# Kernel tuning notes

Hardware: AMD Instinct MI355X
Metric: run time of the kernel (lower is better)

The kernel has to match this reference:

```python
import jax, jax.numpy as jnp
import numpy as np

V, E, H = 100000, 50, 64   # vocab, embedding dim, GRU hidden
B, T = 1024, 200           # batch, max playlist length


def setup_inputs() -> dict:
    key = jax.random.key(0)
    ks = jax.random.split(key, 12)
    ids = jax.random.randint(ks[0], (B, T), 1, V)
    lengths = jax.random.randint(ks[1], (B,), T // 4, T + 1)
    pos = jnp.arange(T)[None, :]
    input_tracks = jnp.where(pos < lengths[:, None], ids, 0)  # 0 = pad (mask_zero)
    s = 0.05
    p = lambda k, shp: jax.random.normal(k, shp, dtype=jnp.float32) * s
    z = lambda shp: jnp.zeros(shp, jnp.float32)
    return {
        "input_tracks": input_tracks,
        "emb": p(ks[2], (V, E)),
        "Wx_f": p(ks[3], (E, 3 * H)), "Wh_f": p(ks[4], (H, 3 * H)),
        "bi_f": z(3 * H), "br_f": z(3 * H),
        "Wx_b": p(ks[5], (E, 3 * H)), "Wh_b": p(ks[6], (H, 3 * H)),
        "bi_b": z(3 * H), "br_b": z(3 * H),
        "Wk": p(ks[7], (2 * H, H)), "bk": z(H),
        "Wq": p(ks[8], (H, H)), "bq": z(H),
        "We": p(ks[9], (H, 1)), "be": z(1),
    }


def _gru(x, mask, Wx, Wh, bi, br):
    """Keras GRU (reset_after=True) with masking; masked steps carry state.
    x: [B,T,E] float, mask: [B,T] bool. Returns (outputs [B,T,H], final state [B,H])."""
    gx = jnp.einsum('bte,eh->bth', x, Wx) + bi  # precompute input projections [B,T,3H]

    def step(h, inp):
        gxt, mt = inp                     # [B,3H], [B]
        gh = h @ Wh + br                  # [B,3H] recurrent projections (with recurrent bias)
        xz, xr, xh = jnp.split(gxt, 3, axis=-1)
        hz, hr, hn = jnp.split(gh, 3, axis=-1)
        zg = jax.nn.sigmoid(xz + hz)
        rg = jax.nn.sigmoid(xr + hr)
        hh = jnp.tanh(xh + rg * hn)
        h_new = zg * h + (1.0 - zg) * hh
        h_new = jnp.where(mt[:, None], h_new, h)  # carry state through padding
        return h_new, h_new

    h0 = jnp.zeros((x.shape[0], Wh.shape[0]), x.dtype)
    hT, outs = jax.lax.scan(step, h0, (gx.transpose(1, 0, 2), mask.T))
    return outs.transpose(1, 0, 2), hT


def reference(input_tracks, emb, Wx_f, Wh_f, bi_f, br_f, Wx_b, Wh_b, bi_b, br_b,
              Wk, bk, Wq, bq, We, be):
    mask = input_tracks != 0                       # [B,T]
    x = emb[input_tracks]                          # [B,T,E]
    out_f, h_f = _gru(x, mask, Wx_f, Wh_f, bi_f, br_f)
    out_b_rev, _ = _gru(x[:, ::-1], mask[:, ::-1], Wx_b, Wh_b, bi_b, br_b)
    out_b = out_b_rev[:, ::-1]
    out = jnp.concatenate([out_f, out_b], axis=-1)  # [B,T,2H]
    keys = out @ Wk + bk                            # [B,T,H]
    query = (h_f @ Wq + bq)[:, None, :]             # [B,1,H]
    energy = jnp.tanh(keys + query) @ We + be       # [B,T,1]
    energy = energy + (1.0 - mask.astype(jnp.float32))[:, :, None] * (-1e9)
    weights = jax.nn.softmax(energy, axis=1)        # softmax over time
    context = jnp.sum(weights * out, axis=1)        # [B,2H]
    return context
```

## Files before the change

kernel.cpp:

```cpp
#include <hip/hip_runtime.h>
#include <hip/hip_bf16.h>

#define VV 100000
#define EE 50
#define HH 64
#define BB 1024
#define TT 200

typedef float v4f __attribute__((ext_vector_type(4)));
typedef float f32x4 __attribute__((ext_vector_type(4)));
typedef short bf16x8 __attribute__((ext_vector_type(8)));

__device__ __forceinline__ float fsig(float x) {
    return 1.f / (1.f + __expf(-x));
}
__device__ __forceinline__ float ftanh(float x) {
    float e = __expf(2.f * x);
    return 1.f - 2.f / (e + 1.f);
}
__device__ __forceinline__ short f2bf(float f) {
    union { float f; unsigned u; } v; v.f = f;
    unsigned r = v.u + 0x7FFFu + ((v.u >> 16) & 1u);
    return (short)(r >> 16);
}

__global__ __launch_bounds__(256) void embw_kernel(
    const float* __restrict__ emb,
    const float* __restrict__ Wx_f, const float* __restrict__ bi_f,
    const float* __restrict__ Wx_b, const float* __restrict__ bi_b,
    float* __restrict__ embW_f, float* __restrict__ embW_b)
{
    const float* Wx = blockIdx.y ? Wx_b : Wx_f;
    const float* bi = blockIdx.y ? bi_b : bi_f;
    float* embW     = blockIdx.y ? embW_b : embW_f;
    __shared__ float wx_lds[EE * 192];
    __shared__ float emb_lds[32 * EE];
    const int tid = threadIdx.x;
    const int v0 = blockIdx.x * 32;
    for (int i = tid; i < EE * 192; i += 256) wx_lds[i] = Wx[i];
    for (int i = tid; i < 32 * EE; i += 256) emb_lds[i] = emb[(size_t)v0 * EE + i];
    __syncthreads();
    const int cg = tid & 63;
    const int rg = tid >> 6;
    float acc[8][3];
    #pragma unroll
    for (int i = 0; i < 8; i++) {
        acc[i][0] = bi[cg];
        acc[i][1] = bi[cg + 64];
        acc[i][2] = bi[cg + 128];
    }
    for (int k = 0; k < EE; k++) {
        const float wx0 = wx_lds[k * 192 + cg];
        const float wx1 = wx_lds[k * 192 + cg + 64];
        const float wx2 = wx_lds[k * 192 + cg + 128];
        #pragma unroll
        for (int i = 0; i < 8; i++) {
            const float ev = emb_lds[(rg * 8 + i) * EE + k];
            acc[i][0] = fmaf(ev, wx0, acc[i][0]);
            acc[i][1] = fmaf(ev, wx1, acc[i][1]);
            acc[i][2] = fmaf(ev, wx2, acc[i][2]);
        }
    }
    #pragma unroll
    for (int i = 0; i < 8; i++) {
        const size_t row = (size_t)(v0 + rg * 8 + i) * 192;
        embW[row + cg]       = acc[i][0];
        embW[row + cg + 64]  = acc[i][1];
        embW[row + cg + 128] = acc[i][2];
    }
}

__device__ __forceinline__ void opaque(v4f& x) {
    float a = x[0], b = x[1], c = x[2], d = x[3];
    asm volatile("" : "+v"(a), "+v"(b), "+v"(c), "+v"(d));
    x[0] = a; x[1] = b; x[2] = c; x[3] = d;
}
#define DECL_W(i) \
    v4f wz##i = {Wh[(4*i+0)*192+j],     Wh[(4*i+1)*192+j],     Wh[(4*i+2)*192+j],     Wh[(4*i+3)*192+j]};     \
    v4f wr##i = {Wh[(4*i+0)*192+64+j],  Wh[(4*i+1)*192+64+j],  Wh[(4*i+2)*192+64+j],  Wh[(4*i+3)*192+64+j]};  \
    v4f wn##i = {Wh[(4*i+0)*192+128+j], Wh[(4*i+1)*192+128+j], Wh[(4*i+2)*192+128+j], Wh[(4*i+3)*192+128+j]}; \
    opaque(wz##i); opaque(wr##i); opaque(wn##i);

#define GSTEP(i) { const v4f hv = h4[i]; \
    aZ = __builtin_elementwise_fma(hv, wz##i, aZ); \
    aR = __builtin_elementwise_fma(hv, wr##i, aR); \
    aN = __builtin_elementwise_fma(hv, wn##i, aN); }

__global__ __launch_bounds__(64, 2) void gru4_kernel(
    const int* __restrict__ ids,
    const float* __restrict__ embW_f, const float* __restrict__ embW_b,
    const float* __restrict__ Wh_f, const float* __restrict__ br_f,
    const float* __restrict__ Wh_b, const float* __restrict__ br_b,
    float* __restrict__ outb,
    float* __restrict__ hf_out)
{
    const int j   = threadIdx.x;
    const int b   = blockIdx.x;
    const int dir = blockIdx.y;
    const float* eW = dir ? embW_b : embW_f;
    const float* Wh = dir ? Wh_b : Wh_f;
    const float* br = dir ? br_b : br_f;

    DECL_W(0)  DECL_W(1)  DECL_W(2)  DECL_W(3)
    DECL_W(4)  DECL_W(5)  DECL_W(6)  DECL_W(7)
    DECL_W(8)  DECL_W(9)  DECL_W(10) DECL_W(11)
    DECL_W(12) DECL_W(13) DECL_W(14) DECL_W(15)
    const float brz = br[j], brr = br[64 + j], brn = br[128 + j];

    __shared__ __align__(16) float h_lds[64];
    __shared__ int ids_lds[TT];
    for (int i = j; i < TT; i += 64) ids_lds[i] = ids[(size_t)b * TT + i];
    h_lds[j] = 0.f;
    float hj = 0.f;
    __syncthreads();

    const int t0 = dir ? (TT - 1) : 0;
    const int dt = dir ? -1 : 1;

    int   id0 = ids_lds[t0];
    float gz0 = eW[(size_t)id0 * 192 + j];
    float gr0 = eW[(size_t)id0 * 192 + 64 + j];
    float gn0 = eW[(size_t)id0 * 192 + 128 + j];
    int   id1 = ids_lds[t0 + dt];
    float gz1 = eW[(size_t)id1 * 192 + j];
    float gr1 = eW[(size_t)id1 * 192 + 64 + j];
    float gn1 = eW[(size_t)id1 * 192 + 128 + j];

    float* obase = outb + (size_t)b * TT * 128 + dir * 64 + j;

    for (int s = 0; s < TT; s++) {
        const int t = t0 + s * dt;
        int id2 = 0; float gz2 = 0.f, gr2 = 0.f, gn2 = 0.f;
        if (s + 2 < TT) {
            id2 = ids_lds[t + 2 * dt];
            gz2 = eW[(size_t)id2 * 192 + j];
            gr2 = eW[(size_t)id2 * 192 + 64 + j];
            gn2 = eW[(size_t)id2 * 192 + 128 + j];
        }
        v4f aZ = {brz, 0.f, 0.f, 0.f};
        v4f aR = {brr, 0.f, 0.f, 0.f};
        v4f aN = {brn, 0.f, 0.f, 0.f};
        const v4f* h4 = (const v4f*)h_lds;
        GSTEP(0)  GSTEP(1)  GSTEP(2)  GSTEP(3)
        GSTEP(4)  GSTEP(5)  GSTEP(6)  GSTEP(7)
        GSTEP(8)  GSTEP(9)  GSTEP(10) GSTEP(11)
        GSTEP(12) GSTEP(13) GSTEP(14) GSTEP(15)
        const float az = (aZ[0] + aZ[1]) + (aZ[2] + aZ[3]);
        const float ar = (aR[0] + aR[1]) + (aR[2] + aR[3]);
        const float an = (aN[0] + aN[1]) + (aN[2] + aN[3]);
        const float z  = fsig(gz0 + az);
        const float r  = fsig(gr0 + ar);
        const float hh = ftanh(gn0 + r * an);
        float hnew = z * hj + (1.f - z) * hh;
        hnew = (id0 != 0) ? hnew : hj;
        hj = hnew;
        h_lds[j] = hj;
        obase[(size_t)t * 128] = hj;
        id0 = id1; gz0 = gz1; gr0 = gr1; gn0 = gn1;
        id1 = id2; gz1 = gz2; gr1 = gr2; gn1 = gn2;
    }
    if (dir == 0) hf_out[(size_t)b * 64 + j] = hj;
}

#define NTILE 13

__global__ __launch_bounds__(256) void attn7_kernel(
    const int* __restrict__ ids,
    const float* __restrict__ outb,
    const float* __restrict__ hf,
    const float* __restrict__ Wk, const float* __restrict__ bk,
    const float* __restrict__ Wq, const float* __restrict__ bq,
    const float* __restrict__ We, const float* __restrict__ be,
    float* __restrict__ ctx)
{
    __shared__ __align__(16) short wk_sw[1024 * 8];
    __shared__ float q_lds[64];
    __shared__ float we_lds[64];
    __shared__ float e_lds[TT];
    __shared__ float part[4][128];
    const int b = blockIdx.x;
    const int tid = threadIdx.x;
    const int w = tid >> 6;
    const int lane = tid & 63;
    const int l15 = lane & 15;
    const int lhi = lane >> 4;

    #pragma unroll
    for (int i = 0; i < 4; i++) {
        const int slot = tid + 256 * i;
        const int s_l15 = slot & 15;
        const int s_nt  = (slot >> 4) & 3;
        const int s_lhi = (slot >> 6) & 3;
        const int s_ks  = slot >> 8;
        const int kbase = 32 * s_ks + 8 * s_lhi;
        const int col   = 16 * s_nt + s_l15;
        bf16x8 v;
        #pragma unroll
        for (int jj = 0; jj < 8; jj++) v[jj] = f2bf(Wk[(size_t)(kbase + jj) * 64 + col]);
        *(bf16x8*)&wk_sw[slot * 8] = v;
    }
    if (tid < 64) {
        float qc = bq[tid];
        const float* hfb = hf + (size_t)b * 64;
        for (int k = 0; k < 64; k++) qc = fmaf(hfb[k], Wq[k * 64 + tid], qc);
        q_lds[tid] = qc;
        we_lds[tid] = We[tid];
    }
    __syncthreads();

    for (int tile = w; tile < NTILE; tile += 4) {
        const int t0 = tile * 16;
        const int t = t0 + l15;
        f32x4 acc[4];
        #pragma unroll
        for (int nt = 0; nt < 4; nt++) { acc[nt][0] = 0.f; acc[nt][1] = 0.f; acc[nt][2] = 0.f; acc[nt][3] = 0.f; }
        #pragma unroll
        for (int ks = 0; ks < 4; ks++) {
            bf16x8 a;
            if (t < TT) {
                const float* p = outb + ((size_t)b * TT + t) * 128 + 32 * ks + 8 * lhi;
                const float4 lo = *(const float4*)p;
                const float4 hi = *(const float4*)(p + 4);
                a[0] = f2bf(lo.x); a[1] = f2bf(lo.y); a[2] = f2bf(lo.z); a[3] = f2bf(lo.w);
                a[4] = f2bf(hi.x); a[5] = f2bf(hi.y); a[6] = f2bf(hi.z); a[7] = f2bf(hi.w);
            } else {
                #pragma unroll
                for (int jj = 0; jj < 8; jj++) a[jj] = 0;
            }
            #pragma unroll
            for (int nt = 0; nt < 4; nt++) {
                const bf16x8 bf = *(const bf16x8*)&wk_sw[(ks * 256 + lhi * 64 + nt * 16 + l15) * 8];
                acc[nt] = __builtin_amdgcn_mfma_f32_16x16x32_bf16(a, bf, acc[nt], 0, 0, 0);
            }
        }
        float ep0 = 0.f, ep1 = 0.f, ep2 = 0.f, ep3 = 0.f;
        #pragma unroll
        for (int nt = 0; nt < 4; nt++) {
            const int c = 16 * nt + l15;
            const float qn = q_lds[c];
            const float wen = we_lds[c];
            ep0 = fmaf(wen, ftanh(acc[nt][0] + qn), ep0);
            ep1 = fmaf(wen, ftanh(acc[nt][1] + qn), ep1);
            ep2 = fmaf(wen, ftanh(acc[nt][2] + qn), ep2);
            ep3 = fmaf(wen, ftanh(acc[nt][3] + qn), ep3);
        }
        #pragma unroll
        for (int off = 1; off < 16; off <<= 1) {
            ep0 += __shfl_xor(ep0, off);
            ep1 += __shfl_xor(ep1, off);
            ep2 += __shfl_xor(ep2, off);
            ep3 += __shfl_xor(ep3, off);
        }
        if (l15 == 0) {
            const int rbase = t0 + 4 * lhi;
            if (rbase + 0 < TT) e_lds[rbase + 0] = ep0;
            if (rbase + 1 < TT) e_lds[rbase + 1] = ep1;
            if (rbase + 2 < TT) e_lds[rbase + 2] = ep2;
            if (rbase + 3 < TT) e_lds[rbase + 3] = ep3;
        }
    }
    __syncthreads();
    if (w == 0) {
        const float bev = be[0];
        for (int t = lane; t < TT; t += 64) {
            float e = e_lds[t] + bev;
            if (ids[(size_t)b * TT + t] == 0) e -= 1e9f;
            e_lds[t] = e;
        }
        float m = -1e30f;
        for (int t = lane; t < TT; t += 64) m = fmaxf(m, e_lds[t]);
        #pragma unroll
        for (int off = 32; off > 0; off >>= 1) m = fmaxf(m, __shfl_xor(m, off));
        float ssum = 0.f;
        for (int t = lane; t < TT; t += 64) { const float v = __expf(e_lds[t] - m); e_lds[t] = v; ssum += v; }
        #pragma unroll
        for (int off = 32; off > 0; off >>= 1) ssum += __shfl_xor(ssum, off);
        const float inv = 1.f / ssum;
        for (int t = lane; t < TT; t += 64) e_lds[t] *= inv;
    }
    __syncthreads();
    float c0 = 0.f, c1 = 0.f;
    for (int t = w; t < TT; t += 4) {
        const float* orow = outb + ((size_t)b * TT + t) * 128;
        const float wt = e_lds[t];
        c0 = fmaf(wt, orow[lane], c0);
        c1 = fmaf(wt, orow[64 + lane], c1);
    }
    part[w][lane] = c0;
    part[w][64 + lane] = c1;
    __syncthreads();
    if (tid < 128)
        ctx[(size_t)b * 128 + tid] = part[0][tid] + part[1][tid] + part[2][tid] + part[3][tid];
}

template<bool USE_EMBW>
__global__ __launch_bounds__(192, 2) void gru_kernel(
    const int* __restrict__ ids,
    const float* __restrict__ embW_f, const float* __restrict__ embW_b,
    const float* __restrict__ emb,
    const float* __restrict__ Wx_f, const float* __restrict__ bi_f,
    const float* __restrict__ Wx_b, const float* __restrict__ bi_b,
    const float* __restrict__ Wh_f, const float* __restrict__ br_f,
    const float* __restrict__ Wh_b, const float* __restrict__ br_b,
    float* __restrict__ outb, float* __restrict__ hf_out)
{
    constexpr int R = 4;
    __shared__ float h_lds[R][64];
    __shared__ float rg_lds[R][64];
    __shared__ float hh_lds[R][64];
    __shared__ int ids_lds[R * TT];
    const int tid = threadIdx.x;
    const int w = tid >> 6;
    const int j = tid & 63;
    const int dir = blockIdx.y;
    const int b0 = blockIdx.x * R;
    const float* embW = dir ? embW_b : embW_f;
    const float* Wh   = dir ? Wh_b : Wh_f;
    const float* br   = dir ? br_b : br_f;
    const float* Wx   = dir ? Wx_b : Wx_f;
    const float* bi   = dir ? bi_b : bi_f;
    const int c = w * 64 + j;

    float whc[64];
    #pragma unroll
    for (int k = 0; k < 64; k++) whc[k] = Wh[k * 192 + c];
    const float brc = br[c];
    float wxc[EE];
    float bic = 0.f;
    if (!USE_EMBW) {
        #pragma unroll
        for (int k = 0; k < EE; k++) wxc[k] = Wx[k * 192 + c];
        bic = bi[c];
    }
    for (int i = tid; i < R * TT; i += 192) ids_lds[i] = ids[(size_t)b0 * TT + i];
    if (w == 0) {
        #pragma unroll
        for (int r = 0; r < R; r++) h_lds[r][j] = 0.f;
    }
    __syncthreads();

    for (int s = 0; s < TT; s++) {
        const int t = dir ? (TT - 1 - s) : s;
        int idv[R];
        float gxv[R], accv[R];
        #pragma unroll
        for (int r = 0; r < R; r++) idv[r] = ids_lds[r * TT + t];
        if (USE_EMBW) {
            #pragma unroll
            for (int r = 0; r < R; r++) gxv[r] = embW[(size_t)idv[r] * 192 + c];
        } else {
            #pragma unroll
            for (int r = 0; r < R; r++) {
                float acc = bic;
                const float* er = emb + (size_t)idv[r] * EE;
                #pragma unroll
                for (int k = 0; k < EE; k++) acc = fmaf(er[k], wxc[k], acc);
                gxv[r] = acc;
            }
        }
        #pragma unroll
        for (int r = 0; r < R; r++) {
            float acc = brc;
            const float4* h4 = (const float4*)(&h_lds[r][0]);
            #pragma unroll
            for (int k4 = 0; k4 < 16; k4++) {
                const float4 hv = h4[k4];
                acc = fmaf(hv.x, whc[4 * k4 + 0], acc);
                acc = fmaf(hv.y, whc[4 * k4 + 1], acc);
                acc = fmaf(hv.z, whc[4 * k4 + 2], acc);
                acc = fmaf(hv.w, whc[4 * k4 + 3], acc);
            }
            accv[r] = acc;
        }
        float zg[R] = {};
        if (w == 1) {
            #pragma unroll
            for (int r = 0; r < R; r++) rg_lds[r][j] = fsig(gxv[r] + accv[r]);
        } else if (w == 0) {
            #pragma unroll
            for (int r = 0; r < R; r++) zg[r] = fsig(gxv[r] + accv[r]);
        }
        __syncthreads();
        if (w == 2) {
            #pragma unroll
            for (int r = 0; r < R; r++)
                hh_lds[r][j] = ftanh(gxv[r] + rg_lds[r][j] * accv[r]);
        }
        __syncthreads();
        if (w == 0) {
            #pragma unroll
            for (int r = 0; r < R; r++) {
                const float hold = h_lds[r][j];
                float hnew = hold;
                if (idv[r] != 0) {
                    const float hh = hh_lds[r][j];
                    hnew = zg[r] * hold + (1.f - zg[r]) * hh;
                }
                h_lds[r][j] = hnew;
                outb[((size_t)(b0 + r) * TT + t) * 128 + dir * 64 + j] = hnew;
            }
        }
        __syncthreads();
    }
    if (dir == 0 && w == 0) {
        #pragma unroll
        for (int r = 0; r < R; r++) hf_out[(size_t)(b0 + r) * 64 + j] = h_lds[r][j];
    }
}

extern "C" void kernel_launch(void* const* d_in, const int* in_sizes, int n_in,
                              void* d_out, int out_size, void* d_ws, size_t ws_size,
                              hipStream_t stream) {
    const int*   ids  = (const int*)d_in[0];
    const float* emb  = (const float*)d_in[1];
    const float* Wx_f = (const float*)d_in[2];
    const float* Wh_f = (const float*)d_in[3];
    const float* bi_f = (const float*)d_in[4];
    const float* br_f = (const float*)d_in[5];
    const float* Wx_b = (const float*)d_in[6];
    const float* Wh_b = (const float*)d_in[7];
    const float* bi_b = (const float*)d_in[8];
    const float* br_b = (const float*)d_in[9];
    const float* Wk   = (const float*)d_in[10];
    const float* bk   = (const float*)d_in[11];
    const float* Wq   = (const float*)d_in[12];
    const float* bq   = (const float*)d_in[13];
    const float* We   = (const float*)d_in[14];
    const float* be   = (const float*)d_in[15];
    float* ctx = (float*)d_out;

    float* ws = (float*)d_ws;
    const size_t embw_elems = (size_t)VV * 192;
    const size_t out_elems  = (size_t)BB * TT * 128;
    const size_t hf_elems   = (size_t)BB * 64;
    const size_t need_embw  = (2 * embw_elems + out_elems + hf_elems) * sizeof(float);
    const bool use_embw = (ws_size >= need_embw);

    float *embW_f = nullptr, *embW_b = nullptr, *outb, *hf;
    if (use_embw) {
        embW_f = ws;
        embW_b = embW_f + embw_elems;
        outb   = embW_b + embw_elems;
        hf     = outb + out_elems;
    } else {
        outb = ws;
        hf   = outb + out_elems;
    }

    if (use_embw) {
        embw_kernel<<<dim3(VV / 32, 2), 256, 0, stream>>>(
            emb, Wx_f, bi_f, Wx_b, bi_b, embW_f, embW_b);
        gru4_kernel<<<dim3(BB, 2), 64, 0, stream>>>(
            ids, embW_f, embW_b, Wh_f, br_f, Wh_b, br_b, outb, hf);
    } else {
        gru_kernel<false><<<dim3(BB / 4, 2), 192, 0, stream>>>(
            ids, embW_f, embW_b, emb, Wx_f, bi_f, Wx_b, bi_b,
            Wh_f, br_f, Wh_b, br_b, outb, hf);
    }
    attn7_kernel<<<BB, 256, 0, stream>>>(ids, outb, hf, Wk, bk, Wq, bq, We, be, ctx);
}
```

Baseline: 313.7 us.

## Split GRU recurrence across four waves with K-partitioned dot products

The recurrent GRU kernel now uses 256 threads per sequence: each wave computes 16 hidden columns and each 16-lane group covers a quarter of the hidden-state reduction, combined with cross-lane shuffles. Hidden state is double-buffered in LDS with a block barrier per time step. This shortens the serial FMA chain per step and reduces per-thread weight registers, at the cost of a per-step barrier, shuffle overhead and redundant gate math in each lane group.

Result: slower. 469.8 us (+49.8%).

```diff
diff --git a/kernel.cpp b/kernel.cpp
--- a/kernel.cpp
+++ b/kernel.cpp
@@ -70,23 +70,7 @@
     }
 }
 
-__device__ __forceinline__ void opaque(v4f& x) {
-    float a = x[0], b = x[1], c = x[2], d = x[3];
-    asm volatile("" : "+v"(a), "+v"(b), "+v"(c), "+v"(d));
-    x[0] = a; x[1] = b; x[2] = c; x[3] = d;
-}
-#define DECL_W(i) \
-    v4f wz##i = {Wh[(4*i+0)*192+j],     Wh[(4*i+1)*192+j],     Wh[(4*i+2)*192+j],     Wh[(4*i+3)*192+j]};     \
-    v4f wr##i = {Wh[(4*i+0)*192+64+j],  Wh[(4*i+1)*192+64+j],  Wh[(4*i+2)*192+64+j],  Wh[(4*i+3)*192+64+j]};  \
-    v4f wn##i = {Wh[(4*i+0)*192+128+j], Wh[(4*i+1)*192+128+j], Wh[(4*i+2)*192+128+j], Wh[(4*i+3)*192+128+j]}; \
-    opaque(wz##i); opaque(wr##i); opaque(wn##i);
-
-#define GSTEP(i) { const v4f hv = h4[i]; \
-    aZ = __builtin_elementwise_fma(hv, wz##i, aZ); \
-    aR = __builtin_elementwise_fma(hv, wr##i, aR); \
-    aN = __builtin_elementwise_fma(hv, wn##i, aN); }
-
-__global__ __launch_bounds__(64, 2) void gru4_kernel(
+__global__ __launch_bounds__(256, 2) void gru7_kernel(
     const int* __restrict__ ids,
     const float* __restrict__ embW_f, const float* __restrict__ embW_b,
     const float* __restrict__ Wh_f, const float* __restrict__ br_f,
@@ -94,23 +78,36 @@
     float* __restrict__ outb,
     float* __restrict__ hf_out)
 {
-    const int j   = threadIdx.x;
-    const int b   = blockIdx.x;
-    const int dir = blockIdx.y;
+    const int tid  = threadIdx.x;
+    const int w    = tid >> 6;
+    const int lane = tid & 63;
+    const int l15  = lane & 15;
+    const int kg   = lane >> 4;
+    const int b    = blockIdx.x;
+    const int dir  = blockIdx.y;
     const float* eW = dir ? embW_b : embW_f;
     const float* Wh = dir ? Wh_b : Wh_f;
     const float* br = dir ? br_b : br_f;
-
-    DECL_W(0)  DECL_W(1)  DECL_W(2)  DECL_W(3)
-    DECL_W(4)  DECL_W(5)  DECL_W(6)  DECL_W(7)
-    DECL_W(8)  DECL_W(9)  DECL_W(10) DECL_W(11)
-    DECL_W(12) DECL_W(13) DECL_W(14) DECL_W(15)
-    const float brz = br[j], brr = br[64 + j], brn = br[128 + j];
-
-    __shared__ __align__(16) float h_lds[64];
+    const int c  = 16 * w + l15;
+    const int k0 = 16 * kg;
+
+    v4f wz[4], wr[4], wn[4];
+    #pragma unroll
+    for (int q = 0; q < 4; q++) {
+        #pragma unroll
+        for (int e = 0; e < 4; e++) {
+            const int k = k0 + 4 * q + e;
+            wz[q][e] = Wh[k * 192 + c];
+            wr[q][e] = Wh[k * 192 + 64 + c];
+            wn[q][e] = Wh[k * 192 + 128 + c];
+        }
+    }
+    const float brz = br[c], brr = br[64 + c], brn = br[128 + c];
+
+    __shared__ __align__(16) float h_lds[2][64];
     __shared__ int ids_lds[TT];
-    for (int i = j; i < TT; i += 64) ids_lds[i] = ids[(size_t)b * TT + i];
-    h_lds[j] = 0.f;
+    for (int i = tid; i < TT; i += 256) ids_lds[i] = ids[(size_t)b * TT + i];
+    if (tid < 64) { h_lds[0][tid] = 0.f; h_lds[1][tid] = 0.f; }
     float hj = 0.f;
     __syncthreads();
 
@@ -118,48 +115,59 @@
     const int dt = dir ? -1 : 1;
 
     int   id0 = ids_lds[t0];
-    float gz0 = eW[(size_t)id0 * 192 + j];
-    float gr0 = eW[(size_t)id0 * 192 + 64 + j];
-    float gn0 = eW[(size_t)id0 * 192 + 128 + j];
+    float gz0 = eW[(size_t)id0 * 192 + c];
+    float gr0 = eW[(size_t)id0 * 192 + 64 + c];
+    float gn0 = eW[(size_t)id0 * 192 + 128 + c];
     int   id1 = ids_lds[t0 + dt];
-    float gz1 = eW[(size_t)id1 * 192 + j];
-    float gr1 = eW[(size_t)id1 * 192 + 64 + j];
-    float gn1 = eW[(size_t)id1 * 192 + 128 + j];
-
-    float* obase = outb + (size_t)b * TT * 128 + dir * 64 + j;
+    float gz1 = eW[(size_t)id1 * 192 + c];
+    float gr1 = eW[(size_t)id1 * 192 + 64 + c];
+    float gn1 = eW[(size_t)id1 * 192 + 128 + c];
+
+    float* obase = outb + (size_t)b * TT * 128 + dir * 64 + c;
+    int cur = 0;
 
     for (int s = 0; s < TT; s++) {
         const int t = t0 + s * dt;
         int id2 = 0; float gz2 = 0.f, gr2 = 0.f, gn2 = 0.f;
         if (s + 2 < TT) {
             id2 = ids_lds[t + 2 * dt];
-            gz2 = eW[(size_t)id2 * 192 + j];
-            gr2 = eW[(size_t)id2 * 192 + 64 + j];
-            gn2 = eW[(size_t)id2 * 192 + 128 + j];
-        }
-        v4f aZ = {brz, 0.f, 0.f, 0.f};
-        v4f aR = {brr, 0.f, 0.f, 0.f};
-        v4f aN = {brn, 0.f, 0.f, 0.f};
-        const v4f* h4 = (const v4f*)h_lds;
-        GSTEP(0)  GSTEP(1)  GSTEP(2)  GSTEP(3)
-        GSTEP(4)  GSTEP(5)  GSTEP(6)  GSTEP(7)
-        GSTEP(8)  GSTEP(9)  GSTEP(10) GSTEP(11)
-        GSTEP(12) GSTEP(13) GSTEP(14) GSTEP(15)
-        const float az = (aZ[0] + aZ[1]) + (aZ[2] + aZ[3]);
-        const float ar = (aR[0] + aR[1]) + (aR[2] + aR[3]);
-        const float an = (aN[0] + aN[1]) + (aN[2] + aN[3]);
-        const float z  = fsig(gz0 + az);
-        const float r  = fsig(gr0 + ar);
-        const float hh = ftanh(gn0 + r * an);
+            gz2 = eW[(size_t)id2 * 192 + c];
+            gr2 = eW[(size_t)id2 * 192 + 64 + c];
+            gn2 = eW[(size_t)id2 * 192 + 128 + c];
+        }
+        const v4f* h4 = (const v4f*)&h_lds[cur][0];
+        v4f aZ = {0.f, 0.f, 0.f, 0.f};
+        v4f aR = {0.f, 0.f, 0.f, 0.f};
+        v4f aN = {0.f, 0.f, 0.f, 0.f};
+        #pragma unroll
+        for (int q = 0; q < 4; q++) {
+            const v4f hv = h4[4 * kg + q];
+            aZ = __builtin_elementwise_fma(hv, wz[q], aZ);
+            aR = __builtin_elementwise_fma(hv, wr[q], aR);
+            aN = __builtin_elementwise_fma(hv, wn[q], aN);
+        }
+        float az = (aZ[0] + aZ[1]) + (aZ[2] + aZ[3]);
+        float ar = (aR[0] + aR[1]) + (aR[2] + aR[3]);
+        float an = (aN[0] + aN[1]) + (aN[2] + aN[3]);
+        az += __shfl_xor(az, 16); az += __shfl_xor(az, 32);
+        ar += __shfl_xor(ar, 16); ar += __shfl_xor(ar, 32);
+        an += __shfl_xor(an, 16); an += __shfl_xor(an, 32);
+        const float z  = fsig(gz0 + az + brz);
+        const float r  = fsig(gr0 + ar + brr);
+        const float hh = ftanh(gn0 + r * (an + brn));
         float hnew = z * hj + (1.f - z) * hh;
         hnew = (id0 != 0) ? hnew : hj;
         hj = hnew;
-        h_lds[j] = hj;
-        obase[(size_t)t * 128] = hj;
+        if (kg == 0) {
+            h_lds[cur ^ 1][c] = hj;
+            obase[(size_t)t * 128] = hj;
+        }
+        cur ^= 1;
+        __syncthreads();
         id0 = id1; gz0 = gz1; gr0 = gr1; gn0 = gn1;
         id1 = id2; gz1 = gz2; gr1 = gr2; gn1 = gn2;
     }
-    if (dir == 0) hf_out[(size_t)b * 64 + j] = hj;
+    if (dir == 0 && kg == 0) hf_out[(size_t)b * 64 + c] = hj;
 }
 
 #define NTILE 13
@@ -450,7 +458,7 @@
     if (use_embw) {
         embw_kernel<<<dim3(VV / 32, 2), 256, 0, stream>>>(
             emb, Wx_f, bi_f, Wx_b, bi_b, embW_f, embW_b);
-        gru4_kernel<<<dim3(BB, 2), 64, 0, stream>>>(
+        gru7_kernel<<<dim3(BB, 2), 256, 0, stream>>>(
             ids, embW_f, embW_b, Wh_f, br_f, Wh_b, br_b, outb, hf);
     } else {
         gru_kernel<false><<<dim3(BB / 4, 2), 192, 0, stream>>>(
```
